# Kernel tuning notes

Hardware: AMD Instinct MI355X
Metric: run time of the kernel (lower is better)

The kernel has to match this reference:

```python
import jax, jax.numpy as jnp
import numpy as np

B, T, C = 16, 512, 768
MULT = 4
D_IN = C * MULT          # 3072
HIDDEN = 1024
N_DATES = 16
STACK_SIZE, STACK_STRIDE = 4, 2
MAX_F = 512
N_MASK_TYPES = 5
N_SESSIONS = 4
SCALE = HIDDEN ** 0.5


def setup_inputs() -> dict:
    key = jax.random.key(0)
    ks = jax.random.split(key, 12)
    inp = {
        "spikes": jax.random.normal(ks[0], (B, T, C), dtype=jnp.float32),
        "spikes_mask": jnp.ones((B, T), dtype=jnp.int64),
        "spikes_timestamp": jax.random.randint(ks[1], (B, T), 0, 255).astype(jnp.int64),
        "date_idx": jax.random.randint(ks[2], (B,), 0, N_DATES).astype(jnp.int64),
        "mask_idx": 1,
        "session_idx": 3,
        # params
        "W_embed": jax.random.normal(ks[3], (N_DATES, D_IN, C), dtype=jnp.float32) * 0.02,
        "b_embed": jax.random.normal(ks[4], (N_DATES, D_IN), dtype=jnp.float32) * 0.02,
        "W_stack": jax.random.normal(ks[5], (HIDDEN, D_IN * STACK_SIZE), dtype=jnp.float32) * 0.02,
        "b_stack": jax.random.normal(ks[6], (HIDDEN,), dtype=jnp.float32) * 0.02,
        "pos_table": jax.random.normal(ks[7], (MAX_F, HIDDEN), dtype=jnp.float32) * 0.02,
        "prompt_table": jax.random.normal(ks[8], (N_MASK_TYPES, HIDDEN), dtype=jnp.float32) * 0.02,
        "session_table": jax.random.normal(ks[9], (N_SESSIONS, HIDDEN), dtype=jnp.float32) * 0.02,
    }
    return inp


def reference(spikes, spikes_mask, spikes_timestamp, date_idx, mask_idx, session_idx,
              W_embed, b_embed, W_stack, b_stack, pos_table, prompt_table, session_table):
    Bb = spikes.shape[0]
    # adapt branch: per-sample expert Linear, done as one gather + batched GEMM
    W = W_embed[date_idx]                      # [B, D_IN, C]
    b = b_embed[date_idx]                      # [B, D_IN]
    x = jnp.einsum('btc,bdc->btd', spikes, W) + b[:, None, :]   # [B, T, D_IN]
    x = jax.nn.gelu(x, approximate=False) * SCALE
    # unfold-based stacking: sliding windows over time
    L = (T - STACK_SIZE) // STACK_STRIDE + 1   # 255
    starts = jnp.arange(L) * STACK_STRIDE
    widx = starts[:, None] + jnp.arange(STACK_SIZE)             # [L, size]
    win = x[:, widx, :]                                         # [B, L, size, D_IN]
    stacked = win.reshape(Bb, L, STACK_SIZE * D_IN)
    x = stacked @ W_stack.T + b_stack                           # [B, L, HIDDEN]
    ts = spikes_timestamp[:, :L]
    mask = jnp.prod(spikes_mask[:, widx], axis=-1)              # [B, L]
    # positional embedding
    x = x + pos_table[ts]
    # prompt token
    x = jnp.concatenate(
        [jnp.broadcast_to(prompt_table[mask_idx][None, None, :], (Bb, 1, HIDDEN)), x], axis=1)
    mask = jnp.pad(mask, ((0, 0), (1, 0)), constant_values=1)
    ts = jnp.concatenate([jnp.zeros((Bb, 1), ts.dtype), ts + 1], axis=1)
    # session token
    x = jnp.concatenate(
        [jnp.broadcast_to(session_table[session_idx][None, None, :], (Bb, 1, HIDDEN)), x], axis=1)
    mask = jnp.pad(mask, ((0, 0), (1, 0)), constant_values=1)
    ts = jnp.concatenate([jnp.zeros((Bb, 1), ts.dtype), ts + 1], axis=1)
    # dropout is identity in eval
    return x, mask, ts
```

## Files before the change

### kernel.cpp

```cpp
#include <hip/hip_runtime.h>
#include <hip/hip_bf16.h>

#define BATCH   16
#define TT      512
#define CC      768
#define D_IN    3072
#define HIDDEN  1024
#define LL      255
#define OUTROWS 257
#define KSTACK  12288
#define N_DATES 16

typedef float f32x4 __attribute__((ext_vector_type(4)));
typedef __bf16 bf16x8 __attribute__((ext_vector_type(8)));
typedef unsigned short u16;

__device__ __forceinline__ u16 f2bf(float f) {
    unsigned u = __builtin_bit_cast(unsigned, f);
    u = (u + 0x7FFFu + ((u >> 16) & 1u)) >> 16;
    return (u16)u;
}

__device__ __forceinline__ bf16x8 lds_read8(const u16* p) {
    return __builtin_bit_cast(bf16x8, *(const uint4*)p);
}

__device__ __forceinline__ void gload16(const u16* g, u16* l) {
    __builtin_amdgcn_global_load_lds(
        (const __attribute__((address_space(1))) void*)g,
        (__attribute__((address_space(3))) void*)l, 16, 0, 0);
}

__global__ __launch_bounds__(256) void cvt_wstack(const float* __restrict__ W, u16* __restrict__ out) {
    size_t i = ((size_t)blockIdx.x * 256 + threadIdx.x) * 4;
    size_t stride = (size_t)gridDim.x * 256 * 4;
    for (; i < (size_t)HIDDEN * KSTACK; i += stride) {
        float4 v = *(const float4*)(W + i);
        ushort4 o = make_ushort4(f2bf(v.x), f2bf(v.y), f2bf(v.z), f2bf(v.w));
        *(ushort4*)(out + i) = o;
    }
}

__global__ __launch_bounds__(256) void cvt_spikes(const float* __restrict__ in, u16* __restrict__ out) {
    size_t i = ((size_t)blockIdx.x * 256 + threadIdx.x) * 4;
    size_t stride = (size_t)gridDim.x * 256 * 4;
    for (; i < (size_t)BATCH * TT * CC; i += stride) {
        float4 v = *(const float4*)(in + i);
        ushort4 o = make_ushort4(f2bf(v.x), f2bf(v.y), f2bf(v.z), f2bf(v.w));
        *(ushort4*)(out + i) = o;
    }
}

__global__ __launch_bounds__(64) void date_flags(const int* __restrict__ date_idx, int* __restrict__ flags) {
    const int tid = threadIdx.x;
    if (tid < N_DATES) flags[tid] = 0;
    __syncthreads();
    if (tid < BATCH) flags[date_idx[tid]] = 1;
}

__global__ __launch_bounds__(256) void cvt_wembed(const float* __restrict__ W,
                                                  const int* __restrict__ flags,
                                                  u16* __restrict__ out) {
    const int date = blockIdx.y;
    if (!flags[date]) return;
    const size_t bofs = (size_t)date * D_IN * CC;
    const size_t i = bofs + ((size_t)blockIdx.x * 256 + threadIdx.x) * 4;
    float4 v = *(const float4*)(W + i);
    ushort4 o = make_ushort4(f2bf(v.x), f2bf(v.y), f2bf(v.z), f2bf(v.w));
    *(ushort4*)(out + i) = o;
}

__global__ __launch_bounds__(512, 2) void gemm1_bf(const u16* __restrict__ spk,
                                                   const u16* __restrict__ wemb,
                                                   const float* __restrict__ b_embed,
                                                   const int* __restrict__ date_idx,
                                                   u16* __restrict__ x1) {
    const int m0 = blockIdx.x * 256;
    const int n0 = blockIdx.y * 256;
    const int bb = blockIdx.z;
    const int date = date_idx[bb];
    const u16* A  = spk  + (size_t)bb   * TT * CC;
    const u16* Bw = wemb + (size_t)date * D_IN * CC;
    const int nt = CC / 64;

    __shared__ u16 Asm[2 * 256 * 64];
    __shared__ u16 Bsm[2 * 256 * 64];

    const int tid  = threadIdx.x;
    const int lane = tid & 63;
    const int wave = tid >> 6;
    const int wm = wave >> 2;
    const int wn = wave & 3;

    const int lrow = lane >> 3;
    const int scol = ((lane & 7) ^ lrow) << 3;

    f32x4 acc[8][4] = {};

    auto STAGE = [&](int k0, int buf) {
        u16* Ad = Asm + buf * (256 * 64);
        u16* Bd = Bsm + buf * (256 * 64);
        #pragma unroll
        for (int i = 0; i < 4; ++i) {
            const int rb = i * 8 + wave;
            const int row = rb * 8 + lrow;
            gload16(A  + (size_t)(m0 + row) * CC + k0 + scol, Ad + rb * 512);
            gload16(Bw + (size_t)(n0 + row) * CC + k0 + scol, Bd + rb * 512);
        }
    };

    STAGE(0, 0);
    STAGE(64, 1);

    for (int t = 0; t < nt; ++t) {
        const int cur = t & 1;
        if (t + 1 < nt) { asm volatile("s_waitcnt vmcnt(8)" ::: "memory"); }
        else            { asm volatile("s_waitcnt vmcnt(0)" ::: "memory"); }
        __builtin_amdgcn_s_barrier();
        asm volatile("" ::: "memory");

        const u16* Ab = Asm + cur * (256 * 64);
        const u16* Bb = Bsm + cur * (256 * 64);
        #pragma unroll
        for (int kk = 0; kk < 64; kk += 32) {
            bf16x8 af[8], bfr[4];
            const int krow = lane & 15;
            const int kcol = kk + ((lane >> 4) << 3);
            #pragma unroll
            for (int i = 0; i < 8; ++i) {
                const int ra = wm * 128 + i * 16 + krow;
                af[i] = lds_read8(&Ab[ra * 64 + (kcol ^ ((ra & 7) << 3))]);
            }
            #pragma unroll
            for (int j = 0; j < 4; ++j) {
                const int rb2 = wn * 64 + j * 16 + krow;
                bfr[j] = lds_read8(&Bb[rb2 * 64 + (kcol ^ ((rb2 & 7) << 3))]);
            }
            #pragma unroll
            for (int i = 0; i < 8; ++i)
                #pragma unroll
                for (int j = 0; j < 4; ++j)
                    acc[i][j] = __builtin_amdgcn_mfma_f32_16x16x32_bf16(af[i], bfr[j], acc[i][j], 0, 0, 0);
        }

        asm volatile("" ::: "memory");
        __builtin_amdgcn_s_barrier();
        asm volatile("" ::: "memory");
        if (t + 2 < nt) STAGE((t + 2) * 64, cur);
    }

    const float* be = b_embed + (size_t)date * D_IN;
    #pragma unroll
    for (int i = 0; i < 8; ++i) {
        #pragma unroll
        for (int j = 0; j < 4; ++j) {
            const int col  = n0 + wn * 64 + j * 16 + (lane & 15);
            const float bias = be[col];
            const int rbase = m0 + wm * 128 + i * 16 + ((lane >> 4) << 2);
            #pragma unroll
            for (int q = 0; q < 4; ++q) {
                float v = acc[i][j][q] + bias;
                float g = 0.5f * v * (1.0f + erff(v * 0.70710678118654752f)) * 32.0f;
                x1[(size_t)bb * TT * D_IN + (size_t)(rbase + q) * D_IN + col] = f2bf(g);
            }
        }
    }
}

__global__ __launch_bounds__(256) void gemm1_f32(const float* __restrict__ spikes,
                                                 const float* __restrict__ W_embed,
                                                 const float* __restrict__ b_embed,
                                                 const int* __restrict__ date_idx,
                                                 u16* __restrict__ x1) {
    const int m0 = blockIdx.x * 128;
    const int n0 = blockIdx.y * 128;
    const int bb = blockIdx.z;
    const int date = date_idx[bb];
    const float* A  = spikes  + (size_t)bb  * TT * CC;
    const float* Bw = W_embed + (size_t)date * D_IN * CC;

    __shared__ u16 As[128 * 64];
    __shared__ u16 Bs[128 * 64];

    const int tid  = threadIdx.x;
    const int lane = tid & 63;
    const int wave = tid >> 6;
    const int wm = wave >> 1, wn = wave & 1;

    f32x4 acc[4][4] = {};

    for (int k0 = 0; k0 < CC; k0 += 64) {
        {
            const int c4 = tid & 15;
            int r = tid >> 4;
            #pragma unroll
            for (int p = 0; p < 8; ++p, r += 16) {
                float4 va = *(const float4*)(A  + (size_t)(m0 + r) * CC + k0 + c4 * 4);
                float4 vb = *(const float4*)(Bw + (size_t)(n0 + r) * CC + k0 + c4 * 4);
                const int col = c4 * 4;
                const int idx = r * 64 + (col ^ ((r & 7) << 3));
                *(ushort4*)(&As[idx]) = make_ushort4(f2bf(va.x), f2bf(va.y), f2bf(va.z), f2bf(va.w));
                *(ushort4*)(&Bs[idx]) = make_ushort4(f2bf(vb.x), f2bf(vb.y), f2bf(vb.z), f2bf(vb.w));
            }
        }
        __syncthreads();
        #pragma unroll
        for (int kk = 0; kk < 64; kk += 32) {
            bf16x8 af[4], bfr[4];
            const int krow = lane & 15;
            const int kcol = kk + ((lane >> 4) << 3);
            #pragma unroll
            for (int i = 0; i < 4; ++i) {
                const int ra = wm * 64 + i * 16 + krow;
                af[i]  = lds_read8(&As[ra * 64 + (kcol ^ ((ra & 7) << 3))]);
                const int rb = wn * 64 + i * 16 + krow;
                bfr[i] = lds_read8(&Bs[rb * 64 + (kcol ^ ((rb & 7) << 3))]);
            }
            #pragma unroll
            for (int i = 0; i < 4; ++i)
                #pragma unroll
                for (int j = 0; j < 4; ++j)
                    acc[i][j] = __builtin_amdgcn_mfma_f32_16x16x32_bf16(af[i], bfr[j], acc[i][j], 0, 0, 0);
        }
        __syncthreads();
    }

    const float* be = b_embed + (size_t)date * D_IN;
    #pragma unroll
    for (int i = 0; i < 4; ++i) {
        #pragma unroll
        for (int j = 0; j < 4; ++j) {
            const int col  = n0 + wn * 64 + j * 16 + (lane & 15);
            const float bias = be[col];
            const int rbase = m0 + wm * 64 + i * 16 + ((lane >> 4) << 2);
            #pragma unroll
            for (int q = 0; q < 4; ++q) {
                float v = acc[i][j][q] + bias;
                float g = 0.5f * v * (1.0f + erff(v * 0.70710678118654752f)) * 32.0f;
                x1[(size_t)bb * TT * D_IN + (size_t)(rbase + q) * D_IN + col] = f2bf(g);
            }
        }
    }
}

template <bool WRITE_PART>
__global__ __launch_bounds__(512, 2) void gemm2(const u16* __restrict__ x1,
                                                const u16* __restrict__ Wbf,
                                                float* __restrict__ part,
                                                const float* __restrict__ b_stack,
                                                const float* __restrict__ pos_table,
                                                const int* __restrict__ tstamp,
                                                float* __restrict__ out,
                                                int KS) {
    const int n0 = blockIdx.x * 256;
    const int ks = blockIdx.y;
    const int bb = blockIdx.z;
    const int KCH  = KSTACK / KS;
    const int kbeg = ks * KCH;
    const int S    = KCH / 32;
    const u16* Xb = x1 + (size_t)bb * TT * D_IN;

    __shared__ u16 Asm[4][128 * 64];
    __shared__ u16 Bsm[4][128 * 64];

    const int tid  = threadIdx.x;
    const int lane = tid & 63;
    const int wave = tid >> 6;
    const int wm = wave >> 2;
    const int wn = wave & 3;

    const int lrow  = lane >> 3;
    const int scol  = ((lane & 7) ^ lrow) << 3;
    const int chalf = scol >> 5;
    const int gk    = scol & 31;

    f32x4 acc[8][4] = {};

    auto STAGE = [&](int slice) {
        const int slot = slice & 3;
        const int k0 = kbeg + slice * 32;
        const int s  = k0 / D_IN;
        const int d0 = k0 % D_IN;
        u16* Ad = Asm[slot];
        u16* Bd = Bsm[slot];
        #pragma unroll
        for (int p = 0; p < 2; ++p) {
            const int rbase = (wave + 8 * p) * 8;
            const int u  = rbase + lrow;
            const int tr = 2 * u + chalf;
            int gl = tr; if (gl > LL - 1) gl = LL - 1;
            gload16(Xb + (size_t)(2 * gl + s) * D_IN + d0 + gk, Ad + rbase * 64);
            gload16(Wbf + (size_t)(n0 + tr) * KSTACK + k0 + gk, Bd + rbase * 64);
        }
    };

    STAGE(0); STAGE(1); STAGE(2);

    const int krow  = lane & 15;
    const int kcol  = (lane >> 4) << 3;
    const int cfrag = (kcol + ((krow & 1) << 5)) ^ ((krow >> 1) << 3);
    const int urow  = krow >> 1;

    for (int ph = 0; ph < S; ++ph) {
        if (ph < S - 2)       { asm volatile("s_waitcnt vmcnt(8)" ::: "memory"); }
        else if (ph == S - 2) { asm volatile("s_waitcnt vmcnt(4)" ::: "memory"); }
        else                  { asm volatile("s_waitcnt vmcnt(0)" ::: "memory"); }
        __builtin_amdgcn_s_barrier();
        asm volatile("" ::: "memory");

        const u16* Ab = Asm[ph & 3];
        const u16* Bb = Bsm[ph & 3];
        bf16x8 af[8], bfr[4];
        #pragma unroll
        for (int i = 0; i < 8; ++i)
            af[i] = lds_read8(&Ab[(wm * 64 + i * 8 + urow) * 64 + cfrag]);
        #pragma unroll
        for (int j = 0; j < 4; ++j)
            bfr[j] = lds_read8(&Bb[(wn * 32 + j * 8 + urow) * 64 + cfrag]);

        if (ph + 3 < S) STAGE(ph + 3);

        __builtin_amdgcn_s_setprio(1);
        #pragma unroll
        for (int i = 0; i < 8; ++i)
            #pragma unroll
            for (int j = 0; j < 4; ++j)
                acc[i][j] = __builtin_amdgcn_mfma_f32_16x16x32_bf16(af[i], bfr[j], acc[i][j], 0, 0, 0);
        __builtin_amdgcn_s_setprio(0);
    }

    if (WRITE_PART) {
        float* pt = part + ((size_t)(ks * BATCH + bb) * 256) * HIDDEN;
        #pragma unroll
        for (int i = 0; i < 8; ++i) {
            #pragma unroll
            for (int j = 0; j < 4; ++j) {
                const int col = n0 + wn * 64 + j * 16 + (lane & 15);
                const int rb  = wm * 128 + i * 16 + ((lane >> 4) << 2);
                #pragma unroll
                for (int q = 0; q < 4; ++q)
                    pt[(size_t)(rb + q) * HIDDEN + col] = acc[i][j][q];
            }
        }
    } else {
        #pragma unroll
        for (int i = 0; i < 8; ++i) {
            #pragma unroll
            for (int j = 0; j < 4; ++j) {
                const int col = n0 + wn * 64 + j * 16 + (lane & 15);
                const int lb  = wm * 128 + i * 16 + ((lane >> 4) << 2);
                #pragma unroll
                for (int q = 0; q < 4; ++q) {
                    const int l = lb + q;
                    if (l < LL) {
                        const int tsv = tstamp[bb * TT + l];
                        float v = acc[i][j][q] + b_stack[col] + pos_table[(size_t)tsv * HIDDEN + col];
                        out[(size_t)bb * OUTROWS * HIDDEN + (size_t)(2 + l) * HIDDEN + col] = v;
                    }
                }
            }
        }
    }
}

__global__ __launch_bounds__(256) void reduce_ep(const float* __restrict__ part,
                                                 const float* __restrict__ b_stack,
                                                 const float* __restrict__ pos_table,
                                                 const int* __restrict__ tstamp,
                                                 float* __restrict__ out,
                                                 int KS) {
    const int idx = blockIdx.x * 256 + threadIdx.x;
    const int c4  = idx & (HIDDEN / 4 - 1);
    const int r   = idx >> 8;
    if (r >= BATCH * LL) return;
    const int l  = r % LL;
    const int bb = r / LL;
    float4 v = make_float4(0.f, 0.f, 0.f, 0.f);
    for (int ks = 0; ks < KS; ++ks) {
        float4 p = *(const float4*)(part + ((size_t)(ks * BATCH + bb) * 256 + l) * HIDDEN + c4 * 4);
        v.x += p.x; v.y += p.y; v.z += p.z; v.w += p.w;
    }
    const int tsv = tstamp[bb * TT + l];
    float4 bs = *(const float4*)(b_stack + c4 * 4);
    float4 ps = *(const float4*)(pos_table + (size_t)tsv * HIDDEN + c4 * 4);
    v.x += bs.x + ps.x; v.y += bs.y + ps.y; v.z += bs.z + ps.z; v.w += bs.w + ps.w;
    *(float4*)(out + ((size_t)bb * OUTROWS + 2 + l) * HIDDEN + c4 * 4) = v;
}

__global__ __launch_bounds__(256) void epilogue_misc(const int* __restrict__ smask,
                                                     const int* __restrict__ tstamp,
                                                     const int* __restrict__ mask_idx_p,
                                                     const int* __restrict__ session_idx_p,
                                                     const float* __restrict__ prompt_table,
                                                     const float* __restrict__ session_table,
                                                     float* __restrict__ out) {
    const int bb = blockIdx.x;
    const int tid = threadIdx.x;
    const int mi = mask_idx_p[0];
    const int si = session_idx_p[0];
    float* xb = out + (size_t)bb * OUTROWS * HIDDEN;
    for (int i = tid; i < HIDDEN; i += 256) {
        xb[i]          = session_table[(size_t)si * HIDDEN + i];
        xb[HIDDEN + i] = prompt_table[(size_t)mi * HIDDEN + i];
    }
    float* maskout = out + (size_t)BATCH * OUTROWS * HIDDEN + (size_t)bb * OUTROWS;
    float* tsout   = out + (size_t)BATCH * OUTROWS * HIDDEN + (size_t)BATCH * OUTROWS + (size_t)bb * OUTROWS;
    for (int j = tid; j < OUTROWS; j += 256) {
        if (j == 0)      { maskout[0] = 1.0f; tsout[0] = 0.0f; }
        else if (j == 1) { maskout[1] = 1.0f; tsout[1] = 1.0f; }
        else {
            const int l = j - 2;
            int m = 1;
            #pragma unroll
            for (int s = 0; s < 4; ++s) m *= smask[bb * TT + 2 * l + s];
            maskout[j] = (float)m;
            tsout[j]   = (float)(tstamp[bb * TT + l] + 2);
        }
    }
}

extern "C" void kernel_launch(void* const* d_in, const int* in_sizes, int n_in,
                              void* d_out, int out_size, void* d_ws, size_t ws_size,
                              hipStream_t stream) {
    const float* spikes      = (const float*)d_in[0];
    const int*   spikes_mask = (const int*)d_in[1];
    const int*   tstamp      = (const int*)d_in[2];
    const int*   date_idx    = (const int*)d_in[3];
    const int*   mask_idx    = (const int*)d_in[4];
    const int*   session_idx = (const int*)d_in[5];
    const float* W_embed     = (const float*)d_in[6];
    const float* b_embed     = (const float*)d_in[7];
    const float* W_stack     = (const float*)d_in[8];
    const float* b_stack     = (const float*)d_in[9];
    const float* pos_table   = (const float*)d_in[10];
    const float* prompt_tab  = (const float*)d_in[11];
    const float* session_tab = (const float*)d_in[12];
    float* out = (float*)d_out;

    const size_t X1_B   = (size_t)BATCH * TT * D_IN * 2;
    const size_t WBF_B  = (size_t)HIDDEN * KSTACK * 2;
    const size_t PART_B = (size_t)BATCH * 256 * HIDDEN * 4;
    const size_t FLAGS_B = 4096;
    const size_t SPK_B  = (size_t)BATCH * TT * CC * 2;
    const size_t WEMB_B = (size_t)N_DATES * D_IN * CC * 2;
    const size_t BASE   = X1_B + WBF_B;
    const size_t UNION_BF = FLAGS_B + SPK_B + WEMB_B;

    u16*   x1    = (u16*)d_ws;
    u16*   Wbf   = (u16*)((char*)d_ws + X1_B);
    int*   flags = (int*)((char*)d_ws + BASE);
    u16*   spkbf = (u16*)((char*)d_ws + BASE + FLAGS_B);
    u16*   wembf = (u16*)((char*)d_ws + BASE + FLAGS_B + SPK_B);
    float* part  = (float*)((char*)d_ws + BASE);

    const bool use_bf = (ws_size >= BASE + UNION_BF);
    int KS = 0;
    if (use_bf) KS = 4;
    else {
        size_t rem = (ws_size > BASE) ? (ws_size - BASE) : 0;
        KS = (int)(rem / PART_B); if (KS > 4) KS = 4;
    }

    cvt_wstack<<<2048, 256, 0, stream>>>(W_stack, Wbf);

    if (use_bf) {
        date_flags<<<1, 64, 0, stream>>>(date_idx, flags);
        cvt_spikes<<<2048, 256, 0, stream>>>(spikes, spkbf);
        cvt_wembed<<<dim3(D_IN * CC / 4 / 256, N_DATES), 256, 0, stream>>>(W_embed, flags, wembf);
        gemm1_bf<<<dim3(TT / 256, D_IN / 256, BATCH), 512, 0, stream>>>(spkbf, wembf, b_embed, date_idx, x1);
    } else {
        gemm1_f32<<<dim3(TT / 128, D_IN / 128, BATCH), 256, 0, stream>>>(spikes, W_embed, b_embed, date_idx, x1);
    }

    if (KS > 0) {
        gemm2<true><<<dim3(HIDDEN / 256, KS, BATCH), 512, 0, stream>>>(x1, Wbf, part, b_stack, pos_table, tstamp, out, KS);
        reduce_ep<<<(BATCH * LL * (HIDDEN / 4) + 255) / 256, 256, 0, stream>>>(part, b_stack, pos_table, tstamp, out, KS);
    } else {
        gemm2<false><<<dim3(HIDDEN / 256, 1, BATCH), 512, 0, stream>>>(x1, Wbf, part, b_stack, pos_table, tstamp, out, 1);
    }
    epilogue_misc<<<BATCH, 256, 0, stream>>>(spikes_mask, tstamp, mask_idx, session_idx,
                                             prompt_tab, session_tab, out);
}
```

Baseline: 246.1 us.

## Prefetch next-stage LDS fragments into registers with 4-slot ring in both GEMMs

```diff
diff --git a/kernel.cpp b/kernel.cpp
--- a/kernel.cpp
+++ b/kernel.cpp
@@ -30,6 +30,33 @@
         (const __attribute__((address_space(1))) void*)g,
         (__attribute__((address_space(3))) void*)l, 16, 0, 0);
 }
+
+#define RING_PHASE(PH, S, CA, CB, NA, NB)                                          \
+    {                                                                              \
+        const int ph_ = (PH);                                                      \
+        if (ph_ + 1 < (S)) {                                                       \
+            if (ph_ + 2 < (S)) { asm volatile("s_waitcnt vmcnt(4)" ::: "memory"); }\
+            else               { asm volatile("s_waitcnt vmcnt(0)" ::: "memory"); }\
+            __builtin_amdgcn_s_barrier();                                          \
+            const u16* Ab_ = Asm[(ph_ + 1) & 3];                                   \
+            const u16* Bb_ = Bsm[(ph_ + 1) & 3];                                   \
+            _Pragma("unroll")                                                      \
+            for (int i_ = 0; i_ < 8; ++i_)                                         \
+                NA[i_] = lds_read8(&Ab_[(wm * 64 + i_ * 8 + urow) * 64 + cfrag]);  \
+            _Pragma("unroll")                                                      \
+            for (int j_ = 0; j_ < 4; ++j_)                                         \
+                NB[j_] = lds_read8(&Bb_[(wn * 32 + j_ * 8 + urow) * 64 + cfrag]);  \
+            if (ph_ + 3 < (S)) STAGE(ph_ + 3);                                     \
+        }                                                                          \
+        __builtin_amdgcn_s_setprio(1);                                             \
+        _Pragma("unroll")                                                          \
+        for (int i_ = 0; i_ < 8; ++i_)                                             \
+            _Pragma("unroll")                                                      \
+            for (int j_ = 0; j_ < 4; ++j_)                                         \
+                acc[i_][j_] = __builtin_amdgcn_mfma_f32_16x16x32_bf16(             \
+                    CA[i_], CB[j_], acc[i_][j_], 0, 0, 0);                         \
+        __builtin_amdgcn_s_setprio(0);                                             \
+    }
 
 __global__ __launch_bounds__(256) void cvt_wstack(const float* __restrict__ W, u16* __restrict__ out) {
     size_t i = ((size_t)blockIdx.x * 256 + threadIdx.x) * 4;
@@ -81,10 +108,10 @@
     const int date = date_idx[bb];
     const u16* A  = spk  + (size_t)bb   * TT * CC;
     const u16* Bw = wemb + (size_t)date * D_IN * CC;
-    const int nt = CC / 64;
-
-    __shared__ u16 Asm[2 * 256 * 64];
-    __shared__ u16 Bsm[2 * 256 * 64];
+    const int S = CC / 32;
+
+    __shared__ u16 Asm[4][128 * 64];
+    __shared__ u16 Bsm[4][128 * 64];
 
     const int tid  = threadIdx.x;
     const int lane = tid & 63;
@@ -92,61 +119,51 @@
     const int wm = wave >> 2;
     const int wn = wave & 3;
 
-    const int lrow = lane >> 3;
-    const int scol = ((lane & 7) ^ lrow) << 3;
+    const int lrow  = lane >> 3;
+    const int scol  = ((lane & 7) ^ lrow) << 3;
+    const int chalf = scol >> 5;
+    const int gk    = scol & 31;
 
     f32x4 acc[8][4] = {};
 
-    auto STAGE = [&](int k0, int buf) {
-        u16* Ad = Asm + buf * (256 * 64);
-        u16* Bd = Bsm + buf * (256 * 64);
-        #pragma unroll
-        for (int i = 0; i < 4; ++i) {
-            const int rb = i * 8 + wave;
-            const int row = rb * 8 + lrow;
-            gload16(A  + (size_t)(m0 + row) * CC + k0 + scol, Ad + rb * 512);
-            gload16(Bw + (size_t)(n0 + row) * CC + k0 + scol, Bd + rb * 512);
+    auto STAGE = [&](int slice) {
+        const int slot = slice & 3;
+        const int k0 = slice * 32;
+        u16* Ad = Asm[slot];
+        u16* Bd = Bsm[slot];
+        #pragma unroll
+        for (int p = 0; p < 2; ++p) {
+            const int rbase = (wave + 8 * p) * 8;
+            const int tr = 2 * (rbase + lrow) + chalf;
+            gload16(A  + (size_t)(m0 + tr) * CC + k0 + gk, Ad + rbase * 64);
+            gload16(Bw + (size_t)(n0 + tr) * CC + k0 + gk, Bd + rbase * 64);
         }
     };
 
-    STAGE(0, 0);
-    STAGE(64, 1);
-
-    for (int t = 0; t < nt; ++t) {
-        const int cur = t & 1;
-        if (t + 1 < nt) { asm volatile("s_waitcnt vmcnt(8)" ::: "memory"); }
-        else            { asm volatile("s_waitcnt vmcnt(0)" ::: "memory"); }
-        __builtin_amdgcn_s_barrier();
-        asm volatile("" ::: "memory");
-
-        const u16* Ab = Asm + cur * (256 * 64);
-        const u16* Bb = Bsm + cur * (256 * 64);
-        #pragma unroll
-        for (int kk = 0; kk < 64; kk += 32) {
-            bf16x8 af[8], bfr[4];
-            const int krow = lane & 15;
-            const int kcol = kk + ((lane >> 4) << 3);
-            #pragma unroll
-            for (int i = 0; i < 8; ++i) {
-                const int ra = wm * 128 + i * 16 + krow;
-                af[i] = lds_read8(&Ab[ra * 64 + (kcol ^ ((ra & 7) << 3))]);
-            }
-            #pragma unroll
-            for (int j = 0; j < 4; ++j) {
-                const int rb2 = wn * 64 + j * 16 + krow;
-                bfr[j] = lds_read8(&Bb[rb2 * 64 + (kcol ^ ((rb2 & 7) << 3))]);
-            }
-            #pragma unroll
-            for (int i = 0; i < 8; ++i)
-                #pragma unroll
-                for (int j = 0; j < 4; ++j)
-                    acc[i][j] = __builtin_amdgcn_mfma_f32_16x16x32_bf16(af[i], bfr[j], acc[i][j], 0, 0, 0);
-        }
-
-        asm volatile("" ::: "memory");
-        __builtin_amdgcn_s_barrier();
-        asm volatile("" ::: "memory");
-        if (t + 2 < nt) STAGE((t + 2) * 64, cur);
+    const int krow  = lane & 15;
+    const int kcol  = (lane >> 4) << 3;
+    const int cfrag = (kcol + ((krow & 1) << 5)) ^ ((krow >> 1) << 3);
+    const int urow  = krow >> 1;
+
+    bf16x8 afA[8], bfA[4], afB[8], bfB[4];
+
+    STAGE(0); STAGE(1); STAGE(2);
+    asm volatile("s_waitcnt vmcnt(8)" ::: "memory");
+    __builtin_amdgcn_s_barrier();
+    {
+        const u16* Ab_ = Asm[0];
+        const u16* Bb_ = Bsm[0];
+        #pragma unroll
+        for (int i = 0; i < 8; ++i)
+            afA[i] = lds_read8(&Ab_[(wm * 64 + i * 8 + urow) * 64 + cfrag]);
+        #pragma unroll
+        for (int j = 0; j < 4; ++j)
+            bfA[j] = lds_read8(&Bb_[(wn * 32 + j * 8 + urow) * 64 + cfrag]);
+    }
+
+    for (int t = 0; t < S; t += 2) {
+        RING_PHASE(t,     S, afA, bfA, afB, bfB);
+        RING_PHASE(t + 1, S, afB, bfB, afA, bfA);
     }
 
     const float* be = b_embed + (size_t)date * D_IN;
@@ -286,47 +303,36 @@
         #pragma unroll
         for (int p = 0; p < 2; ++p) {
             const int rbase = (wave + 8 * p) * 8;
-            const int u  = rbase + lrow;
-            const int tr = 2 * u + chalf;
-            int gl = tr; if (gl > LL - 1) gl = LL - 1;
-            gload16(Xb + (size_t)(2 * gl + s) * D_IN + d0 + gk, Ad + rbase * 64);
+            const int tr = 2 * (rbase + lrow) + chalf;
+            gload16(Xb + (size_t)(2 * tr + s) * D_IN + d0 + gk, Ad + rbase * 64);
             gload16(Wbf + (size_t)(n0 + tr) * KSTACK + k0 + gk, Bd + rbase * 64);
         }
     };
-
-    STAGE(0); STAGE(1); STAGE(2);
 
     const int krow  = lane & 15;
     const int kcol  = (lane >> 4) << 3;
     const int cfrag = (kcol + ((krow & 1) << 5)) ^ ((krow >> 1) << 3);
     const int urow  = krow >> 1;
 
-    for (int ph = 0; ph < S; ++ph) {
-        if (ph < S - 2)       { asm volatile("s_waitcnt vmcnt(8)" ::: "memory"); }
-        else if (ph == S - 2) { asm volatile("s_waitcnt vmcnt(4)" ::: "memory"); }
-        else                  { asm volatile("s_waitcnt vmcnt(0)" ::: "memory"); }
-        __builtin_amdgcn_s_barrier();
-        asm volatile("" ::: "memory");
-
-        const u16* Ab = Asm[ph & 3];
-        const u16* Bb = Bsm[ph & 3];
-        bf16x8 af[8], bfr[4];
+    bf16x8 afA[8], bfA[4], afB[8], bfB[4];
+
+    STAGE(0); STAGE(1); STAGE(2);
+    asm volatile("s_waitcnt vmcnt(8)" ::: "memory");
+    __builtin_amdgcn_s_barrier();
+    {
+        const u16* Ab_ = Asm[0];
+        const u16* Bb_ = Bsm[0];
         #pragma unroll
         for (int i = 0; i < 8; ++i)
-            af[i] = lds_read8(&Ab[(wm * 64 + i * 8 + urow) * 64 + cfrag]);
+            afA[i] = lds_read8(&Ab_[(wm * 64 + i * 8 + urow) * 64 + cfrag]);
         #pragma unroll
         for (int j = 0; j < 4; ++j)
-            bfr[j] = lds_read8(&Bb[(wn * 32 + j * 8 + urow) * 64 + cfrag]);
-
-        if (ph + 3 < S) STAGE(ph + 3);
-
-        __builtin_amdgcn_s_setprio(1);
-        #pragma unroll
-        for (int i = 0; i < 8; ++i)
-            #pragma unroll
-            for (int j = 0; j < 4; ++j)
-                acc[i][j] = __builtin_amdgcn_mfma_f32_16x16x32_bf16(af[i], bfr[j], acc[i][j], 0, 0, 0);
-        __builtin_amdgcn_s_setprio(0);
+            bfA[j] = lds_read8(&Bb_[(wn * 32 + j * 8 + urow) * 64 + cfrag]);
+    }
+
+    for (int t = 0; t < S; t += 2) {
+        RING_PHASE(t,     S, afA, bfA, afB, bfB);
+        RING_PHASE(t + 1, S, afB, bfB, afA, bfA);
     }
 
     if (WRITE_PART) {
```

After: 255.7 us. 1.04x slower.

## Retile both GEMMs to 256-thread 256x128 blocks with triple buffering and XCD swizzle

Applied to the files above, without the earlier changes.

```diff
diff --git a/kernel.cpp b/kernel.cpp
--- a/kernel.cpp
+++ b/kernel.cpp
@@ -70,83 +70,92 @@
     *(ushort4*)(out + i) = o;
 }
 
-__global__ __launch_bounds__(512, 2) void gemm1_bf(const u16* __restrict__ spk,
+
+__global__ __launch_bounds__(256, 4) void gemm1_bf(const u16* __restrict__ spk,
                                                    const u16* __restrict__ wemb,
                                                    const float* __restrict__ b_embed,
                                                    const int* __restrict__ date_idx,
                                                    u16* __restrict__ x1) {
-    const int m0 = blockIdx.x * 256;
-    const int n0 = blockIdx.y * 256;
-    const int bb = blockIdx.z;
+    const int nwg = 2 * 24 * BATCH;
+    const int cpx = nwg / 8;
+    const int f   = blockIdx.x;
+    const int swz = (f & 7) * cpx + (f >> 3);
+    const int bb  = swz / 48;
+    const int rem = swz % 48;
+    const int m0  = (rem / 24) * 256;
+    const int n0  = (rem % 24) * 128;
+
     const int date = date_idx[bb];
     const u16* A  = spk  + (size_t)bb   * TT * CC;
     const u16* Bw = wemb + (size_t)date * D_IN * CC;
-    const int nt = CC / 64;
-
-    __shared__ u16 Asm[2 * 256 * 64];
-    __shared__ u16 Bsm[2 * 256 * 64];
+    const int S = CC / 32;
+
+    __shared__ u16 Asm[3][128 * 64];
+    __shared__ u16 Bsm[3][64 * 64];
 
     const int tid  = threadIdx.x;
     const int lane = tid & 63;
     const int wave = tid >> 6;
-    const int wm = wave >> 2;
-    const int wn = wave & 3;
-
-    const int lrow = lane >> 3;
-    const int scol = ((lane & 7) ^ lrow) << 3;
+    const int wm = wave >> 1;
+    const int wn = wave & 1;
+
+    const int lrow  = lane >> 3;
+    const int scol  = ((lane & 7) ^ lrow) << 3;
+    const int chalf = scol >> 5;
+    const int gk    = scol & 31;
 
     f32x4 acc[8][4] = {};
 
-    auto STAGE = [&](int k0, int buf) {
-        u16* Ad = Asm + buf * (256 * 64);
-        u16* Bd = Bsm + buf * (256 * 64);
-        #pragma unroll
-        for (int i = 0; i < 4; ++i) {
-            const int rb = i * 8 + wave;
-            const int row = rb * 8 + lrow;
-            gload16(A  + (size_t)(m0 + row) * CC + k0 + scol, Ad + rb * 512);
-            gload16(Bw + (size_t)(n0 + row) * CC + k0 + scol, Bd + rb * 512);
+    auto STAGE = [&](int slice, int slot) {
+        const int k0 = slice * 32;
+        u16* Ad = Asm[slot];
+        u16* Bd = Bsm[slot];
+        #pragma unroll
+        for (int p = 0; p < 4; ++p) {
+            const int rbase = (wave + 4 * p) * 8;
+            const int tr = 2 * (rbase + lrow) + chalf;
+            gload16(A + (size_t)(m0 + tr) * CC + k0 + gk, Ad + rbase * 64);
+        }
+        #pragma unroll
+        for (int p = 0; p < 2; ++p) {
+            const int rbase = (wave + 4 * p) * 8;
+            const int tr = 2 * (rbase + lrow) + chalf;
+            gload16(Bw + (size_t)(n0 + tr) * CC + k0 + gk, Bd + rbase * 64);
         }
     };
 
-    STAGE(0, 0);
-    STAGE(64, 1);
-
-    for (int t = 0; t < nt; ++t) {
-        const int cur = t & 1;
-        if (t + 1 < nt) { asm volatile("s_waitcnt vmcnt(8)" ::: "memory"); }
-        else            { asm volatile("s_waitcnt vmcnt(0)" ::: "memory"); }
+    const int krow  = lane & 15;
+    const int kcol  = (lane >> 4) << 3;
+    const int cfrag = (kcol + ((krow & 1) << 5)) ^ ((krow >> 1) << 3);
+    const int urow  = krow >> 1;
+
+    STAGE(0, 0); STAGE(1, 1);
+    int cur = 0;
+    for (int t = 0; t < S; ++t) {
+        if (t + 1 < S) { asm volatile("s_waitcnt vmcnt(6)" ::: "memory"); }
+        else           { asm volatile("s_waitcnt vmcnt(0)" ::: "memory"); }
         __builtin_amdgcn_s_barrier();
-        asm volatile("" ::: "memory");
-
-        const u16* Ab = Asm + cur * (256 * 64);
-        const u16* Bb = Bsm + cur * (256 * 64);
-        #pragma unroll
-        for (int kk = 0; kk < 64; kk += 32) {
-            bf16x8 af[8], bfr[4];
-            const int krow = lane & 15;
-            const int kcol = kk + ((lane >> 4) << 3);
-            #pragma unroll
-            for (int i = 0; i < 8; ++i) {
-                const int ra = wm * 128 + i * 16 + krow;
-                af[i] = lds_read8(&Ab[ra * 64 + (kcol ^ ((ra & 7) << 3))]);
-            }
-            #pragma unroll
-            for (int j = 0; j < 4; ++j) {
-                const int rb2 = wn * 64 + j * 16 + krow;
-                bfr[j] = lds_read8(&Bb[rb2 * 64 + (kcol ^ ((rb2 & 7) << 3))]);
-            }
-            #pragma unroll
-            for (int i = 0; i < 8; ++i)
-                #pragma unroll
-                for (int j = 0; j < 4; ++j)
-                    acc[i][j] = __builtin_amdgcn_mfma_f32_16x16x32_bf16(af[i], bfr[j], acc[i][j], 0, 0, 0);
-        }
-
-        asm volatile("" ::: "memory");
-        __builtin_amdgcn_s_barrier();
-        asm volatile("" ::: "memory");
-        if (t + 2 < nt) STAGE((t + 2) * 64, cur);
+        const u16* Ab = Asm[cur];
+        const u16* Bb = Bsm[cur];
+        bf16x8 af[8], bfr[4];
+        #pragma unroll
+        for (int i = 0; i < 8; ++i)
+            af[i] = lds_read8(&Ab[(wm * 64 + i * 8 + urow) * 64 + cfrag]);
+        #pragma unroll
+        for (int j = 0; j < 4; ++j)
+            bfr[j] = lds_read8(&Bb[(wn * 32 + j * 8 + urow) * 64 + cfrag]);
+        if (t + 2 < S) {
+            const int slot2 = (cur + 2 >= 3) ? cur - 1 : cur + 2;
+            STAGE(t + 2, slot2);
+        }
+        __builtin_amdgcn_s_setprio(1);
+        #pragma unroll
+        for (int i = 0; i < 8; ++i)
+            #pragma unroll
+            for (int j = 0; j < 4; ++j)
+                acc[i][j] = __builtin_amdgcn_mfma_f32_16x16x32_bf16(af[i], bfr[j], acc[i][j], 0, 0, 0);
+        __builtin_amdgcn_s_setprio(0);
+        cur = (cur + 1 >= 3) ? 0 : cur + 1;
     }
 
     const float* be = b_embed + (size_t)date * D_IN;
@@ -244,7 +253,7 @@
 }
 
 template <bool WRITE_PART>
-__global__ __launch_bounds__(512, 2) void gemm2(const u16* __restrict__ x1,
+__global__ __launch_bounds__(256, 4) void gemm2(const u16* __restrict__ x1,
                                                 const u16* __restrict__ Wbf,
                                                 float* __restrict__ part,
                                                 const float* __restrict__ b_stack,
@@ -252,22 +261,28 @@
                                                 const int* __restrict__ tstamp,
                                                 float* __restrict__ out,
                                                 int KS) {
-    const int n0 = blockIdx.x * 256;
-    const int ks = blockIdx.y;
-    const int bb = blockIdx.z;
+    const int nwg = 8 * KS * BATCH;
+    const int cpx = nwg / 8;
+    const int f   = blockIdx.x;
+    const int swz = (f & 7) * cpx + (f >> 3);
+    const int bb  = swz / (8 * KS);
+    const int rem = swz % (8 * KS);
+    const int ks  = rem / 8;
+    const int n0  = (rem % 8) * 128;
+
     const int KCH  = KSTACK / KS;
     const int kbeg = ks * KCH;
     const int S    = KCH / 32;
     const u16* Xb = x1 + (size_t)bb * TT * D_IN;
 
-    __shared__ u16 Asm[4][128 * 64];
-    __shared__ u16 Bsm[4][128 * 64];
+    __shared__ u16 Asm[3][128 * 64];
+    __shared__ u16 Bsm[3][64 * 64];
 
     const int tid  = threadIdx.x;
     const int lane = tid & 63;
     const int wave = tid >> 6;
-    const int wm = wave >> 2;
-    const int wn = wave & 3;
+    const int wm = wave >> 1;
+    const int wn = wave & 1;
 
     const int lrow  = lane >> 3;
     const int scol  = ((lane & 7) ^ lrow) << 3;
@@ -276,40 +291,39 @@
 
     f32x4 acc[8][4] = {};
 
-    auto STAGE = [&](int slice) {
-        const int slot = slice & 3;
+    auto STAGE = [&](int slice, int slot) {
         const int k0 = kbeg + slice * 32;
         const int s  = k0 / D_IN;
         const int d0 = k0 % D_IN;
         u16* Ad = Asm[slot];
         u16* Bd = Bsm[slot];
         #pragma unroll
+        for (int p = 0; p < 4; ++p) {
+            const int rbase = (wave + 4 * p) * 8;
+            const int tr = 2 * (rbase + lrow) + chalf;
+            gload16(Xb + (size_t)(2 * tr + s) * D_IN + d0 + gk, Ad + rbase * 64);
+        }
+        #pragma unroll
         for (int p = 0; p < 2; ++p) {
-            const int rbase = (wave + 8 * p) * 8;
-            const int u  = rbase + lrow;
-            const int tr = 2 * u + chalf;
-            int gl = tr; if (gl > LL - 1) gl = LL - 1;
-            gload16(Xb + (size_t)(2 * gl + s) * D_IN + d0 + gk, Ad + rbase * 64);
+            const int rbase = (wave + 4 * p) * 8;
+            const int tr = 2 * (rbase + lrow) + chalf;
             gload16(Wbf + (size_t)(n0 + tr) * KSTACK + k0 + gk, Bd + rbase * 64);
         }
     };
-
-    STAGE(0); STAGE(1); STAGE(2);
 
     const int krow  = lane & 15;
     const int kcol  = (lane >> 4) << 3;
     const int cfrag = (kcol + ((krow & 1) << 5)) ^ ((krow >> 1) << 3);
     const int urow  = krow >> 1;
 
-    for (int ph = 0; ph < S; ++ph) {
-        if (ph < S - 2)       { asm volatile("s_waitcnt vmcnt(8)" ::: "memory"); }
-        else if (ph == S - 2) { asm volatile("s_waitcnt vmcnt(4)" ::: "memory"); }
-        else                  { asm volatile("s_waitcnt vmcnt(0)" ::: "memory"); }
+    STAGE(0, 0); STAGE(1, 1);
+    int cur = 0;
+    for (int t = 0; t < S; ++t) {
+        if (t + 1 < S) { asm volatile("s_waitcnt vmcnt(6)" ::: "memory"); }
+        else           { asm volatile("s_waitcnt vmcnt(0)" ::: "memory"); }
         __builtin_amdgcn_s_barrier();
-        asm volatile("" ::: "memory");
-
-        const u16* Ab = Asm[ph & 3];
-        const u16* Bb = Bsm[ph & 3];
+        const u16* Ab = Asm[cur];
+        const u16* Bb = Bsm[cur];
         bf16x8 af[8], bfr[4];
         #pragma unroll
         for (int i = 0; i < 8; ++i)
@@ -317,9 +331,10 @@
         #pragma unroll
         for (int j = 0; j < 4; ++j)
             bfr[j] = lds_read8(&Bb[(wn * 32 + j * 8 + urow) * 64 + cfrag]);
-
-        if (ph + 3 < S) STAGE(ph + 3);
-
+        if (t + 2 < S) {
+            const int slot2 = (cur + 2 >= 3) ? cur - 1 : cur + 2;
+            STAGE(t + 2, slot2);
+        }
         __builtin_amdgcn_s_setprio(1);
         #pragma unroll
         for (int i = 0; i < 8; ++i)
@@ -327,6 +342,7 @@
             for (int j = 0; j < 4; ++j)
                 acc[i][j] = __builtin_amdgcn_mfma_f32_16x16x32_bf16(af[i], bfr[j], acc[i][j], 0, 0, 0);
         __builtin_amdgcn_s_setprio(0);
+        cur = (cur + 1 >= 3) ? 0 : cur + 1;
     }
 
     if (WRITE_PART) {
@@ -467,16 +483,16 @@
         date_flags<<<1, 64, 0, stream>>>(date_idx, flags);
         cvt_spikes<<<2048, 256, 0, stream>>>(spikes, spkbf);
         cvt_wembed<<<dim3(D_IN * CC / 4 / 256, N_DATES), 256, 0, stream>>>(W_embed, flags, wembf);
-        gemm1_bf<<<dim3(TT / 256, D_IN / 256, BATCH), 512, 0, stream>>>(spkbf, wembf, b_embed, date_idx, x1);
+        gemm1_bf<<<2 * 24 * BATCH, 256, 0, stream>>>(spkbf, wembf, b_embed, date_idx, x1);
     } else {
         gemm1_f32<<<dim3(TT / 128, D_IN / 128, BATCH), 256, 0, stream>>>(spikes, W_embed, b_embed, date_idx, x1);
     }
 
     if (KS > 0) {
-        gemm2<true><<<dim3(HIDDEN / 256, KS, BATCH), 512, 0, stream>>>(x1, Wbf, part, b_stack, pos_table, tstamp, out, KS);
+        gemm2<true><<<8 * KS * BATCH, 256, 0, stream>>>(x1, Wbf, part, b_stack, pos_table, tstamp, out, KS);
         reduce_ep<<<(BATCH * LL * (HIDDEN / 4) + 255) / 256, 256, 0, stream>>>(part, b_stack, pos_table, tstamp, out, KS);
     } else {
-        gemm2<false><<<dim3(HIDDEN / 256, 1, BATCH), 512, 0, stream>>>(x1, Wbf, part, b_stack, pos_table, tstamp, out, 1);
+        gemm2<false><<<8 * 1 * BATCH, 256, 0, stream>>>(x1, Wbf, part, b_stack, pos_table, tstamp, out, 1);
     }
     epilogue_misc<<<BATCH, 256, 0, stream>>>(spikes_mask, tstamp, mask_idx, session_idx,
                                              prompt_tab, session_tab, out);
```

Result: slower. 273.5 us (+11.1%).
